# Performance work log

Hardware: AMD Instinct MI355X
Metric: run time of the kernel (lower is better)

Reference implementation:

```python
import jax, jax.numpy as jnp
import numpy as np

T_STEPS, B, I, H = 512, 64, 128, 256
LAST_K, RSIZE = 16, 32


def _xavier(key, shape):
    fan_out, fan_in = shape[0], shape[-1]
    std = (2.0 / (fan_in + fan_out)) ** 0.5
    return (std * jax.random.normal(key, shape)).astype(jnp.float32)


def setup_inputs() -> dict:
    key = jax.random.key(0)
    ks = jax.random.split(key, 8)
    inp = {"x": jax.random.normal(ks[0], (T_STEPS, B, I), dtype=jnp.float32)}
    for n, k in zip(["Wf", "Wi", "Wo", "Wg"], ks[1:5]):
        inp[n + "_w"] = _xavier(k, (H, H + I))
        inp[n + "_b"] = jnp.zeros((H,), jnp.float32)
    inp["Ua_w"] = _xavier(ks[5], (H, H))
    inp["Va_w"] = _xavier(ks[6], (H, H))
    inp["v"] = _xavier(ks[7], (1, H))
    return inp


def _forward(x, Wf_w, Wf_b, Wi_w, Wi_b, Wo_w, Wo_b, Wg_w, Wg_b, Ua_w, Va_w, v):
    T = x.shape[0]
    vv = v[0]  # [H]
    neg_inf = jnp.float32(-jnp.inf)

    def lstm(st, ct, xt):
        inp = jnp.concatenate([st, xt], axis=1)  # [B, H+I], order (hidden, input) as in torch cat((st, x), 1)
        ft = jax.nn.sigmoid(inp @ Wf_w.T + Wf_b)
        it = jax.nn.sigmoid(inp @ Wi_w.T + Wi_b)
        ot = jax.nn.sigmoid(inp @ Wo_w.T + Wo_b)
        gt = jnp.tanh(inp @ Wg_w.T + Wg_b)
        ct = ft * ct + it * gt
        return ot * jnp.tanh(ct), ct

    # ---- step 0 (reset path): st = zero hidden, no attention ----
    st0 = jnp.zeros((B, H), jnp.float32)
    h0, ct0 = lstm(st0, jnp.zeros((B, H), jnp.float32), x[0])
    mem0 = jnp.zeros((LAST_K, B, H), jnp.float32).at[-1].set(h0)  # ring of last_k hiddens (zeros = not yet filled)
    carry0 = (st0, ct0, mem0,
              jnp.zeros((RSIZE, B, H), jnp.float32),   # long_mem buckets
              jnp.full((RSIZE, B), neg_inf),            # long_mask (-inf = empty bucket)
              jnp.zeros((T, B), jnp.float32),           # long_scores (detached accumulator)
              jnp.zeros((B, RSIZE), jnp.float32),       # buck_scores
              jnp.zeros((B,), jnp.int32))               # per-sample bucket fill count

    def body(carry, tx):
        st, ct, mem, long_mem, long_mask, long_scores, buck, fill = carry
        t, xt = tx
        slots = jnp.arange(LAST_K)
        short_valid = slots >= (LAST_K - t)  # slot j holds h_{t-LAST_K+j}; valid iff time >= 0
        # ---- additive attention over short memory + long-term buckets ----
        q = st @ Va_w.T                              # [B,H]
        Uahs = mem @ Ua_w.T                          # [LAST_K,B,H]
        long_uas = long_mem @ Ua_w.T                 # [RSIZE,B,H]
        es = jnp.einsum('kbh,h->kb', jnp.tanh(q[None] + Uahs), vv)
        es = jnp.where(short_valid[:, None], es, neg_inf)
        es_long = jnp.einsum('rbh,h->rb', jnp.tanh(q[None] + long_uas), vv) + long_mask
        alphas = jax.nn.softmax(jnp.concatenate([es, es_long], 0), axis=0)  # [LAST_K+RSIZE,B]
        # accumulate detached attention mass onto absolute-time scores
        det_a = jax.lax.stop_gradient(alphas[:LAST_K])
        times = jnp.clip(t - LAST_K + slots, 0, T - 1)
        long_scores = long_scores.at[times].add(jnp.where(short_valid[:, None], det_a, 0.0))
        comb = jnp.concatenate([mem, long_mem], 0)   # [LAST_K+RSIZE,B,H]
        ct_att = jnp.einsum('nb,nbh->bh', alphas, comb)
        st = 0.5 * (mem[-1] + ct_att)                # comb_hs[-1-rsize] == previous hidden
        # ---- LSTM gating ----
        hidden, ct = lstm(st, ct, xt)
        # ---- bucket insert / argmin-replace (active once t >= LAST_K) ----
        cand = mem[0]                                # h_{t-LAST_K} == memory[0]
        cand_score = jax.lax.stop_gradient(
            jax.lax.dynamic_index_in_dim(long_scores, jnp.clip(t - LAST_K, 0, T - 1), 0, keepdims=False))  # [B]
        minp = jnp.argmin(buck, axis=1)              # [B], first-min like torch.argmin
        min_val = jnp.take_along_axis(buck, minp[:, None], axis=1)[:, 0]
        full = fill >= RSIZE
        addpos = jnp.where(full, minp, fill)
        do_upd = (t >= LAST_K) & (jnp.logical_not(full) | (cand_score > min_val))
        onehot = (jnp.arange(RSIZE)[None, :] == addpos[:, None]) & do_upd[:, None]  # [B,RSIZE]
        sel = onehot.T                               # [RSIZE,B]
        long_mem = jnp.where(sel[:, :, None], cand[None], long_mem)
        long_mask = jnp.where(sel, 0.0, long_mask)
        buck = jnp.where(onehot, cand_score[:, None], buck)
        fill = fill + (do_upd & jnp.logical_not(full)).astype(jnp.int32)
        # ---- push hidden into short-memory ring ----
        mem = jnp.concatenate([mem[1:], hidden[None]], 0)
        return (st, ct, mem, long_mem, long_mask, long_scores, buck, fill), hidden

    ts = jnp.arange(1, T)
    _, hs = jax.lax.scan(jax.checkpoint(body), carry0, (ts, x[1:]))
    return jnp.concatenate([h0[None], hs], 0)  # [T,B,H]


def reference(x, Wf_w, Wf_b, Wi_w, Wi_b, Wo_w, Wo_b, Wg_w, Wg_b, Ua_w, Va_w, v):
    return _forward(x, Wf_w, Wf_b, Wi_w, Wi_b, Wo_w, Wo_b, Wg_w, Wg_b, Ua_w, Va_w, v)
```

## Files before the change

kernel.cpp:

```cpp
#include <hip/hip_runtime.h>
#include <hip/hip_fp16.h>

#define T_STEPS 512
#define NB      64
#define NI      128
#define NH      256
#define LK      16
#define RS      32
#define NS      (LK + RS)

#define WP_OFF   0
#define VAP8_OFF 786432
#define UAP8_OFF 917504
#define LRAW_OFF 1048576
#define LUA_OFF  3145728
#define GX_OFF   5242880
#define WS_NEED  (GX_OFF + (size_t)T_STEPS * NB * NH * 8)

typedef _Float16 half2v __attribute__((ext_vector_type(2)));

__device__ __forceinline__ float hdot(unsigned int w, unsigned int s, float c) {
    return __builtin_amdgcn_fdot2(__builtin_bit_cast(half2v, w),
                                  __builtin_bit_cast(half2v, s), c, false);
}

__device__ __forceinline__ float fsig(float x) {
    return __builtin_amdgcn_rcpf(1.0f + __expf(-x));
}
__device__ __forceinline__ float ftanh(float x) {
    x = fminf(15.0f, fmaxf(-15.0f, x));
    float e = __expf(2.0f * x);
    return (e - 1.0f) * __builtin_amdgcn_rcpf(e + 1.0f);
}

__global__ void prep_weights(const float* __restrict__ Wf, const float* __restrict__ Wi,
                             const float* __restrict__ Wo, const float* __restrict__ Wg,
                             const float* __restrict__ Ua, const float* __restrict__ Va,
                             unsigned char* __restrict__ ws) {
    int e = blockIdx.x * 256 + threadIdx.x;
    if (e < 49152) {
        int h = e & 255, k2 = e >> 8, k = 2 * k2;
        uint4 w; __half2 t;
        t = __floats2half2_rn(Wf[h * 384 + k], Wf[h * 384 + k + 1]); w.x = *(unsigned int*)&t;
        t = __floats2half2_rn(Wi[h * 384 + k], Wi[h * 384 + k + 1]); w.y = *(unsigned int*)&t;
        t = __floats2half2_rn(Wo[h * 384 + k], Wo[h * 384 + k + 1]); w.z = *(unsigned int*)&t;
        t = __floats2half2_rn(Wg[h * 384 + k], Wg[h * 384 + k + 1]); w.w = *(unsigned int*)&t;
        ((uint4*)(ws + WP_OFF))[e] = w;
    } else {
        int e2 = e - 49152;
        const float* S = (e2 < 8192) ? Va : Ua;
        int e3 = e2 & 8191;
        int h = e3 & 255, j = e3 >> 8, k = 8 * j;
        uint4 w; __half2 t;
        t = __floats2half2_rn(S[h * 256 + k + 0], S[h * 256 + k + 1]); w.x = *(unsigned int*)&t;
        t = __floats2half2_rn(S[h * 256 + k + 2], S[h * 256 + k + 3]); w.y = *(unsigned int*)&t;
        t = __floats2half2_rn(S[h * 256 + k + 4], S[h * 256 + k + 5]); w.z = *(unsigned int*)&t;
        t = __floats2half2_rn(S[h * 256 + k + 6], S[h * 256 + k + 7]); w.w = *(unsigned int*)&t;
        ((uint4*)(ws + VAP8_OFF))[e2] = w;
    }
}

__global__ __launch_bounds__(256) void gx_gemm(const float* __restrict__ x,
                                               unsigned char* __restrict__ ws) {
    const int t = blockIdx.x, bg = blockIdx.y, tid = threadIdx.x;
    const uint4* __restrict__ WP = (const uint4*)(ws + WP_OFF);
    uint2* __restrict__ GX = (uint2*)(ws + GX_OFF);
    __shared__ float s_xx[16 * 128];
    const float* xb = x + ((size_t)t * NB + bg * 16) * NI;
#pragma unroll
    for (int r = 0; r < 8; ++r) s_xx[tid + 256 * r] = xb[tid + 256 * r];
    __syncthreads();
    const int h = tid;
    float acc[16][4];
#pragma unroll
    for (int bb = 0; bb < 16; ++bb) { acc[bb][0] = acc[bb][1] = acc[bb][2] = acc[bb][3] = 0.f; }
    for (int k2 = 128; k2 < 192; ++k2) {
        uint4 w = WP[k2 * NH + h];
        float2 wf = __half22float2(*(const __half2*)&w.x);
        float2 wi = __half22float2(*(const __half2*)&w.y);
        float2 wo = __half22float2(*(const __half2*)&w.z);
        float2 wg = __half22float2(*(const __half2*)&w.w);
        int kk = 2 * k2 - 256;
#pragma unroll
        for (int bb = 0; bb < 16; ++bb) {
            float2 xv = *(const float2*)(s_xx + bb * 128 + kk);
            acc[bb][0] += wf.x * xv.x + wf.y * xv.y;
            acc[bb][1] += wi.x * xv.x + wi.y * xv.y;
            acc[bb][2] += wo.x * xv.x + wo.y * xv.y;
            acc[bb][3] += wg.x * xv.x + wg.y * xv.y;
        }
    }
#pragma unroll
    for (int bb = 0; bb < 16; ++bb) {
        __half2 p0 = __floats2half2_rn(acc[bb][0], acc[bb][1]);
        __half2 p1 = __floats2half2_rn(acc[bb][2], acc[bb][3]);
        uint2 u; u.x = *(unsigned int*)&p0; u.y = *(unsigned int*)&p1;
        GX[((size_t)t * NB + bg * 16 + bb) * NH + h] = u;
    }
}

template <int USE_GX>
__global__ __launch_bounds__(1024, 1) void rel_lstm(
    const float* __restrict__ x,
    const float* __restrict__ bf_g, const float* __restrict__ bi_g,
    const float* __restrict__ bo_g, const float* __restrict__ bg_g,
    const float* __restrict__ vv_g,
    unsigned char* __restrict__ ws, float* __restrict__ out) {
    const int tid = threadIdx.x;
    const int b   = blockIdx.x;
    const int wv  = tid >> 6;
    const int ln  = tid & 63;
    const int h16 = (wv << 4) | (ln & 15);
    const int kc  = ln >> 4;

    const uint4* __restrict__ WP   = (const uint4*)(ws + WP_OFF);
    const uint4* __restrict__ VaP8 = (const uint4*)(ws + VAP8_OFF);
    const uint4* __restrict__ UaP8 = (const uint4*)(ws + UAP8_OFF);
    const uint2* __restrict__ GX   = (const uint2*)(ws + GX_OFF);
    float* __restrict__ lraw = (float*)(ws + LRAW_OFF) + b * (RS * NH);
    float* __restrict__ lua  = (float*)(ws + LUA_OFF)  + b * (RS * NH);

    __shared__ __align__(16) _Float16 s_in_h[NH + NI];
    __shared__ __align__(16) _Float16 s_hid_h[NH];
    __shared__ __align__(16) float s_q[NH];
    __shared__ __align__(16) float s_v[NH];
    __shared__ __align__(16) float s_mem[LK][NH];
    __shared__ __align__(16) float s_memua[LK][NH + 8];
    __shared__ float s_es[NS], s_al[NS];
    __shared__ float s_scores[T_STEPS];
    __shared__ float s_mask[RS], s_buck[RS];
    __shared__ float s_minv;
    __shared__ int s_minp, s_fill, s_upd, s_pos;

    for (int i = tid; i < LK * NH; i += 1024) ((float*)s_mem)[i] = 0.f;
    for (int i = tid; i < LK * (NH + 8); i += 1024) ((float*)s_memua)[i] = 0.f;
    if (tid < T_STEPS) s_scores[tid] = 0.f;
    if (tid < NH) s_v[tid] = vv_g[tid];
    if (tid < (NH + NI) / 2) ((unsigned int*)s_in_h)[tid] = 0u;
    if (tid < RS) { s_mask[tid] = -1e30f; s_buck[tid] = 0.f; }
    if (tid == 0) { s_fill = 0; s_upd = 0; s_pos = 0; s_minv = 0.f; s_minp = 0; }
    float bfv = 0.f, biv = 0.f, bov = 0.f, bgv = 0.f;
    if (kc == 0) { bfv = bf_g[h16]; biv = bi_g[h16]; bov = bo_g[h16]; bgv = bg_g[h16]; }
    if (!USE_GX && tid < 64) {
        float2 xv = ((const float2*)(x + (size_t)b * NI))[tid];
        __half2 hx = __floats2half2_rn(xv.x, xv.y);
        ((unsigned int*)s_in_h)[NH / 2 + tid] = *(unsigned int*)&hx;
    }
    float ct = 0.f;
    int base = 0;
    __syncthreads();

    for (int t = 0; t < T_STEPS; ++t) {
        float evA = 0.f, evB = 0.f;
        if (t > 0) {
            {
                const uint4* P   = (wv < 8) ? VaP8 : UaP8;
                const uint4* SRC = (wv < 8) ? (const uint4*)s_in_h : (const uint4*)s_hid_h;
                const int hh = ((wv & 7) << 5) | (ln & 31);
                const int ch = ln >> 5;
                float acc = 0.f;
#pragma unroll 8
                for (int jj = 0; jj < 16; ++jj) {
                    int j = (ch << 4) | jj;
                    uint4 w = P[(j << 8) + hh];
                    uint4 s = SRC[j];
                    acc = hdot(w.x, s.x, acc);
                    acc = hdot(w.y, s.y, acc);
                    acc = hdot(w.z, s.z, acc);
                    acc = hdot(w.w, s.w, acc);
                }
                acc += __shfl_xor(acc, 32, 64);
                if (ch == 0) {
                    if (wv < 8) s_q[hh] = acc;
                    else        s_memua[(base + LK - 1) & (LK - 1)][hh] = acc;
                }
                if (!USE_GX && tid < 64) {
                    float2 xv = ((const float2*)(x + ((size_t)t * NB + b) * NI))[tid];
                    __half2 hx = __floats2half2_rn(xv.x, xv.y);
                    ((unsigned int*)s_in_h)[NH / 2 + tid] = *(unsigned int*)&hx;
                }
            }
            __syncthreads();
            if (tid < 768) {
                const int row = tid >> 4, l = tid & 15;
                bool skip;
                const float* ua;
                if (row < LK) { skip = row < LK - t; ua = s_memua[(base + row) & (LK - 1)]; }
                else          { skip = s_mask[row - LK] < -1e29f; ua = lua + (row - LK) * NH; }
                float esv = -1e30f;
                if (!skip) {
                    float p = 0.f;
#pragma unroll
                    for (int jj = 0; jj < 4; ++jj) {
                        int hh = (l << 2) + (jj << 6);
                        float4 q4 = *(const float4*)(s_q + hh);
                        float4 v4 = *(const float4*)(s_v + hh);
                        float4 u4 = *(const float4*)(ua + hh);
                        p += v4.x * ftanh(q4.x + u4.x);
                        p += v4.y * ftanh(q4.y + u4.y);
                        p += v4.z * ftanh(q4.z + u4.z);
                        p += v4.w * ftanh(q4.w + u4.w);
                    }
                    p += __shfl_xor(p, 1, 16);
                    p += __shfl_xor(p, 2, 16);
                    p += __shfl_xor(p, 4, 16);
                    p += __shfl_xor(p, 8, 16);
                    esv = p;
                }
                if (l == 0) s_es[row] = esv;
            } else if (tid >= 960 && tid < 992) {
                int l = tid - 960;
                float v = s_buck[l]; int idx = l;
#pragma unroll
                for (int off = 1; off < 32; off <<= 1) {
                    float v2 = __shfl_xor(v, off, 32);
                    int  i2 = __shfl_xor(idx, off, 32);
                    if (v2 < v || (v2 == v && i2 < idx)) { v = v2; idx = i2; }
                }
                if (l == 0) { s_minv = v; s_minp = idx; }
            }
            __syncthreads();
            if (tid < 64) {
                float e = (tid < NS) ? s_es[tid] : -1e30f;
                float m = e;
#pragma unroll
                for (int off = 32; off; off >>= 1) m = fmaxf(m, __shfl_xor(m, off, 64));
                float a = (tid < NS) ? __expf(e - m) : 0.f;
                float ssum = a;
#pragma unroll
                for (int off = 32; off; off >>= 1) ssum += __shfl_xor(ssum, off, 64);
                float al = a * __builtin_amdgcn_rcpf(ssum);
                if (tid < NS) s_al[tid] = al;
                float cs = 0.f;
                if (tid < LK) {
                    int time = t - LK + tid;
                    if (time >= 0) {
                        float ns = s_scores[time] + al;
                        s_scores[time] = ns;
                        cs = ns;
                    }
                }
                if (tid == 0) {
                    int upd = 0, pos = 0;
                    if (t >= LK) {
                        int fill = s_fill;
                        bool full = fill >= RS;
                        upd = (!full) || (cs > s_minv);
                        pos = full ? s_minp : fill;
                        if (upd) { s_mask[pos] = 0.f; s_buck[pos] = cs; if (!full) s_fill = fill + 1; }
                    }
                    s_upd = upd; s_pos = pos;
                }
            }
            __syncthreads();
            {
                float catt = 0.f;
                const int n0 = kc * 12;
#pragma unroll
                for (int n = n0; n < n0 + 12; ++n) {
                    float a = s_al[n];
                    if (n < LK) catt += a * s_mem[(base + n) & (LK - 1)][h16];
                    else if (a != 0.f) catt += a * lraw[(n - LK) * NH + h16];
                }
                catt += __shfl_xor(catt, 16, 64);
                catt += __shfl_xor(catt, 32, 64);
                if (kc == 1 && s_upd) {
                    int p0 = base & (LK - 1);
                    evA = s_mem[p0][h16];
                    evB = s_memua[p0][h16];
                }
                if (kc == 0) {
                    float stv = 0.5f * (s_mem[(base + LK - 1) & (LK - 1)][h16] + catt);
                    s_in_h[h16] = (_Float16)stv;
                }
            }
            __syncthreads();
        }
        {
            uint2 gx = {0u, 0u};
            if (USE_GX && kc == 0) gx = GX[((size_t)t * NB + b) * NH + h16];
            constexpr int KP = USE_GX ? 32 : 48;
            const unsigned int* S2 = (const unsigned int*)s_in_h;
            float af = 0.f, ai = 0.f, ao = 0.f, ag = 0.f;
            const int lo = kc * KP;
#pragma unroll 8
            for (int k2 = lo; k2 < lo + KP; ++k2) {
                uint4 w = WP[(k2 << 8) + h16];
                unsigned int s2 = S2[k2];
                af = hdot(w.x, s2, af);
                ai = hdot(w.y, s2, ai);
                ao = hdot(w.z, s2, ao);
                ag = hdot(w.w, s2, ag);
            }
            af += __shfl_xor(af, 16, 64); af += __shfl_xor(af, 32, 64);
            ai += __shfl_xor(ai, 16, 64); ai += __shfl_xor(ai, 32, 64);
            ao += __shfl_xor(ao, 16, 64); ao += __shfl_xor(ao, 32, 64);
            ag += __shfl_xor(ag, 16, 64); ag += __shfl_xor(ag, 32, 64);
            if (kc == 0) {
                float pf = af + bfv, pi = ai + biv, po = ao + bov, pg = ag + bgv;
                if (USE_GX) {
                    float2 fi = __half22float2(*(const __half2*)&gx.x);
                    float2 og = __half22float2(*(const __half2*)&gx.y);
                    pf += fi.x; pi += fi.y; po += og.x; pg += og.y;
                }
                float f  = fsig(pf);
                float ii = fsig(pi);
                float o  = fsig(po);
                float g  = ftanh(pg);
                ct = f * ct + ii * g;
                float hid = o * ftanh(ct);
                out[((size_t)t * NB + b) * NH + h16] = hid;
                s_mem[base & (LK - 1)][h16] = hid;
                s_hid_h[h16] = (_Float16)hid;
            } else if (kc == 1 && s_upd) {
                lraw[s_pos * NH + h16] = evA;
                lua[s_pos * NH + h16]  = evB;
            }
        }
        base++;
        __syncthreads();
    }
}

extern "C" void kernel_launch(void* const* d_in, const int* in_sizes, int n_in,
                              void* d_out, int out_size, void* d_ws, size_t ws_size,
                              hipStream_t stream) {
    const float* x  = (const float*)d_in[0];
    const float* Wf = (const float*)d_in[1];
    const float* bf = (const float*)d_in[2];
    const float* Wi = (const float*)d_in[3];
    const float* bi = (const float*)d_in[4];
    const float* Wo = (const float*)d_in[5];
    const float* bo = (const float*)d_in[6];
    const float* Wg = (const float*)d_in[7];
    const float* bg = (const float*)d_in[8];
    const float* Ua = (const float*)d_in[9];
    const float* Va = (const float*)d_in[10];
    const float* vv = (const float*)d_in[11];
    unsigned char* ws = (unsigned char*)d_ws;
    float* out = (float*)d_out;

    prep_weights<<<256, 256, 0, stream>>>(Wf, Wi, Wo, Wg, Ua, Va, ws);
    if (ws_size >= WS_NEED) {
        gx_gemm<<<dim3(T_STEPS, 4), 256, 0, stream>>>(x, ws);
        rel_lstm<1><<<NB, 1024, 0, stream>>>(x, bf, bi, bo, bg, vv, ws, out);
    } else {
        rel_lstm<0><<<NB, 1024, 0, stream>>>(x, bf, bi, bo, bg, vv, ws, out);
    }
}
```

Before: 5.917 ms.

## Move long-memory buffers to LDS and compute softmax redundantly per wave

The per-block long-memory buffers (raw hiddens and their Ua projections) move from global workspace into shared memory, so the attention score and context reads no longer go to global memory. Every wave now computes the softmax itself and broadcasts the weights through shuffles. This removes the s_al array and one block-wide barrier per timestep. The GX prefetch and eviction-candidate reads are also hoisted earlier so their latency overlaps other work. The cost is 64KB more LDS, redundant softmax work in all 16 waves, and a fully unrolled projection loop.

```diff
diff --git a/kernel.cpp b/kernel.cpp
--- a/kernel.cpp
+++ b/kernel.cpp
@@ -12,8 +12,6 @@
 #define WP_OFF   0
 #define VAP8_OFF 786432
 #define UAP8_OFF 917504
-#define LRAW_OFF 1048576
-#define LUA_OFF  3145728
 #define GX_OFF   5242880
 #define WS_NEED  (GX_OFF + (size_t)T_STEPS * NB * NH * 8)
 
@@ -117,8 +115,6 @@
     const uint4* __restrict__ VaP8 = (const uint4*)(ws + VAP8_OFF);
     const uint4* __restrict__ UaP8 = (const uint4*)(ws + UAP8_OFF);
     const uint2* __restrict__ GX   = (const uint2*)(ws + GX_OFF);
-    float* __restrict__ lraw = (float*)(ws + LRAW_OFF) + b * (RS * NH);
-    float* __restrict__ lua  = (float*)(ws + LUA_OFF)  + b * (RS * NH);
 
     __shared__ __align__(16) _Float16 s_in_h[NH + NI];
     __shared__ __align__(16) _Float16 s_hid_h[NH];
@@ -126,7 +122,9 @@
     __shared__ __align__(16) float s_v[NH];
     __shared__ __align__(16) float s_mem[LK][NH];
     __shared__ __align__(16) float s_memua[LK][NH + 8];
-    __shared__ float s_es[NS], s_al[NS];
+    __shared__ __align__(16) float s_lraw[RS * NH];
+    __shared__ __align__(16) float s_lua[RS * NH];
+    __shared__ float s_es[NS];
     __shared__ float s_scores[T_STEPS];
     __shared__ float s_mask[RS], s_buck[RS];
     __shared__ float s_minv;
@@ -134,6 +132,7 @@
 
     for (int i = tid; i < LK * NH; i += 1024) ((float*)s_mem)[i] = 0.f;
     for (int i = tid; i < LK * (NH + 8); i += 1024) ((float*)s_memua)[i] = 0.f;
+    for (int i = tid; i < RS * NH; i += 1024) { s_lraw[i] = 0.f; s_lua[i] = 0.f; }
     if (tid < T_STEPS) s_scores[tid] = 0.f;
     if (tid < NH) s_v[tid] = vv_g[tid];
     if (tid < (NH + NI) / 2) ((unsigned int*)s_in_h)[tid] = 0u;
@@ -152,6 +151,8 @@
 
     for (int t = 0; t < T_STEPS; ++t) {
         float evA = 0.f, evB = 0.f;
+        uint2 gx = {0u, 0u};
+        if (USE_GX && kc == 0) gx = GX[((size_t)t * NB + b) * NH + h16];
         if (t > 0) {
             {
                 const uint4* P   = (wv < 8) ? VaP8 : UaP8;
@@ -159,7 +160,7 @@
                 const int hh = ((wv & 7) << 5) | (ln & 31);
                 const int ch = ln >> 5;
                 float acc = 0.f;
-#pragma unroll 8
+#pragma unroll
                 for (int jj = 0; jj < 16; ++jj) {
                     int j = (ch << 4) | jj;
                     uint4 w = P[(j << 8) + hh];
@@ -174,6 +175,11 @@
                     if (wv < 8) s_q[hh] = acc;
                     else        s_memua[(base + LK - 1) & (LK - 1)][hh] = acc;
                 }
+                if (kc == 1) {
+                    int p0 = base & (LK - 1);
+                    evA = s_mem[p0][h16];
+                    evB = s_memua[p0][h16];
+                }
                 if (!USE_GX && tid < 64) {
                     float2 xv = ((const float2*)(x + ((size_t)t * NB + b) * NI))[tid];
                     __half2 hx = __floats2half2_rn(xv.x, xv.y);
@@ -186,7 +192,7 @@
                 bool skip;
                 const float* ua;
                 if (row < LK) { skip = row < LK - t; ua = s_memua[(base + row) & (LK - 1)]; }
-                else          { skip = s_mask[row - LK] < -1e29f; ua = lua + (row - LK) * NH; }
+                else          { skip = s_mask[row - LK] < -1e29f; ua = s_lua + (row - LK) * NH; }
                 float esv = -1e30f;
                 if (!skip) {
                     float p = 0.f;
@@ -220,55 +226,48 @@
                 if (l == 0) { s_minv = v; s_minp = idx; }
             }
             __syncthreads();
-            if (tid < 64) {
-                float e = (tid < NS) ? s_es[tid] : -1e30f;
+            {
+                float e = (ln < NS) ? s_es[ln] : -1e30f;
                 float m = e;
 #pragma unroll
                 for (int off = 32; off; off >>= 1) m = fmaxf(m, __shfl_xor(m, off, 64));
-                float a = (tid < NS) ? __expf(e - m) : 0.f;
+                float a = (ln < NS) ? __expf(e - m) : 0.f;
                 float ssum = a;
 #pragma unroll
                 for (int off = 32; off; off >>= 1) ssum += __shfl_xor(ssum, off, 64);
                 float al = a * __builtin_amdgcn_rcpf(ssum);
-                if (tid < NS) s_al[tid] = al;
-                float cs = 0.f;
-                if (tid < LK) {
-                    int time = t - LK + tid;
-                    if (time >= 0) {
-                        float ns = s_scores[time] + al;
-                        s_scores[time] = ns;
-                        cs = ns;
+                if (wv == 0) {
+                    float cs = 0.f;
+                    if (ln < LK) {
+                        int time = t - LK + ln;
+                        if (time >= 0) {
+                            float ns = s_scores[time] + al;
+                            s_scores[time] = ns;
+                            cs = ns;
+                        }
                     }
-                }
-                if (tid == 0) {
-                    int upd = 0, pos = 0;
-                    if (t >= LK) {
-                        int fill = s_fill;
-                        bool full = fill >= RS;
-                        upd = (!full) || (cs > s_minv);
-                        pos = full ? s_minp : fill;
-                        if (upd) { s_mask[pos] = 0.f; s_buck[pos] = cs; if (!full) s_fill = fill + 1; }
+                    if (ln == 0) {
+                        int upd = 0, pos = 0;
+                        if (t >= LK) {
+                            int fill = s_fill;
+                            bool full = fill >= RS;
+                            upd = (!full) || (cs > s_minv);
+                            pos = full ? s_minp : fill;
+                            if (upd) { s_mask[pos] = 0.f; s_buck[pos] = cs; if (!full) s_fill = fill + 1; }
+                        }
+                        s_upd = upd; s_pos = pos;
                     }
-                    s_upd = upd; s_pos = pos;
-                }
-            }
-            __syncthreads();
-            {
+                }
                 float catt = 0.f;
                 const int n0 = kc * 12;
 #pragma unroll
                 for (int n = n0; n < n0 + 12; ++n) {
-                    float a = s_al[n];
-                    if (n < LK) catt += a * s_mem[(base + n) & (LK - 1)][h16];
-                    else if (a != 0.f) catt += a * lraw[(n - LK) * NH + h16];
+                    float a2 = __shfl(al, n);
+                    if (n < LK) catt += a2 * s_mem[(base + n) & (LK - 1)][h16];
+                    else if (a2 != 0.f) catt += a2 * s_lraw[(n - LK) * NH + h16];
                 }
                 catt += __shfl_xor(catt, 16, 64);
                 catt += __shfl_xor(catt, 32, 64);
-                if (kc == 1 && s_upd) {
-                    int p0 = base & (LK - 1);
-                    evA = s_mem[p0][h16];
-                    evB = s_memua[p0][h16];
-                }
                 if (kc == 0) {
                     float stv = 0.5f * (s_mem[(base + LK - 1) & (LK - 1)][h16] + catt);
                     s_in_h[h16] = (_Float16)stv;
@@ -277,8 +276,6 @@
             __syncthreads();
         }
         {
-            uint2 gx = {0u, 0u};
-            if (USE_GX && kc == 0) gx = GX[((size_t)t * NB + b) * NH + h16];
             constexpr int KP = USE_GX ? 32 : 48;
             const unsigned int* S2 = (const unsigned int*)s_in_h;
             float af = 0.f, ai = 0.f, ao = 0.f, ag = 0.f;
@@ -313,8 +310,8 @@
                 s_mem[base & (LK - 1)][h16] = hid;
                 s_hid_h[h16] = (_Float16)hid;
             } else if (kc == 1 && s_upd) {
-                lraw[s_pos * NH + h16] = evA;
-                lua[s_pos * NH + h16]  = evB;
+                s_lraw[s_pos * NH + h16] = evA;
+                s_lua[s_pos * NH + h16]  = evB;
             }
         }
         base++;
```

New measurement: 6.094 ms. 1.03x slower.

## Keep long-memory buckets in LDS, prefetch GX early, use nontemporal weight loads

Applied to the files above, without the earlier changes.

Moves the per-sample long-memory bucket arrays (raw hiddens and their Ua projections) from global workspace into shared memory. This removes global-memory round trips inside the sequential per-step critical path. It also issues the GX gate-input load at the top of each step so its latency overlaps the attention phase, and hoists the evicted-slot reads earlier. Weight loads switch to nontemporal loads. The cost is about 64KB of extra LDS per block, which must still fit, and a cache-policy change on weight reads that are reused every step.

```diff
diff --git a/kernel.cpp b/kernel.cpp
--- a/kernel.cpp
+++ b/kernel.cpp
@@ -12,12 +12,23 @@
 #define WP_OFF   0
 #define VAP8_OFF 786432
 #define UAP8_OFF 917504
-#define LRAW_OFF 1048576
-#define LUA_OFF  3145728
 #define GX_OFF   5242880
 #define WS_NEED  (GX_OFF + (size_t)T_STEPS * NB * NH * 8)
 
 typedef _Float16 half2v __attribute__((ext_vector_type(2)));
+typedef unsigned int u32x4 __attribute__((ext_vector_type(4)));
+typedef unsigned int u32x2 __attribute__((ext_vector_type(2)));
+
+__device__ __forceinline__ u32x4 ntl4(const void* p) {
+    return __builtin_nontemporal_load((const u32x4*)p);
+}
+__device__ __forceinline__ u32x2 ntl2(const void* p) {
+    return __builtin_nontemporal_load((const u32x2*)p);
+}
+__device__ __forceinline__ float2 h2f2(unsigned int u) {
+    __half2 h = *(__half2*)&u;
+    return __half22float2(h);
+}
 
 __device__ __forceinline__ float hdot(unsigned int w, unsigned int s, float c) {
     return __builtin_amdgcn_fdot2(__builtin_bit_cast(half2v, w),
@@ -117,8 +128,6 @@
     const uint4* __restrict__ VaP8 = (const uint4*)(ws + VAP8_OFF);
     const uint4* __restrict__ UaP8 = (const uint4*)(ws + UAP8_OFF);
     const uint2* __restrict__ GX   = (const uint2*)(ws + GX_OFF);
-    float* __restrict__ lraw = (float*)(ws + LRAW_OFF) + b * (RS * NH);
-    float* __restrict__ lua  = (float*)(ws + LUA_OFF)  + b * (RS * NH);
 
     __shared__ __align__(16) _Float16 s_in_h[NH + NI];
     __shared__ __align__(16) _Float16 s_hid_h[NH];
@@ -126,6 +135,8 @@
     __shared__ __align__(16) float s_v[NH];
     __shared__ __align__(16) float s_mem[LK][NH];
     __shared__ __align__(16) float s_memua[LK][NH + 8];
+    __shared__ __align__(16) float s_lraw[RS * NH];
+    __shared__ __align__(16) float s_lua[RS * NH];
     __shared__ float s_es[NS], s_al[NS];
     __shared__ float s_scores[T_STEPS];
     __shared__ float s_mask[RS], s_buck[RS];
@@ -134,6 +145,7 @@
 
     for (int i = tid; i < LK * NH; i += 1024) ((float*)s_mem)[i] = 0.f;
     for (int i = tid; i < LK * (NH + 8); i += 1024) ((float*)s_memua)[i] = 0.f;
+    for (int i = tid; i < RS * NH; i += 1024) { s_lraw[i] = 0.f; s_lua[i] = 0.f; }
     if (tid < T_STEPS) s_scores[tid] = 0.f;
     if (tid < NH) s_v[tid] = vv_g[tid];
     if (tid < (NH + NI) / 2) ((unsigned int*)s_in_h)[tid] = 0u;
@@ -152,6 +164,8 @@
 
     for (int t = 0; t < T_STEPS; ++t) {
         float evA = 0.f, evB = 0.f;
+        u32x2 gx = {0u, 0u};
+        if (USE_GX && kc == 0) gx = ntl2(&GX[((size_t)t * NB + b) * NH + h16]);
         if (t > 0) {
             {
                 const uint4* P   = (wv < 8) ? VaP8 : UaP8;
@@ -162,7 +176,7 @@
 #pragma unroll 8
                 for (int jj = 0; jj < 16; ++jj) {
                     int j = (ch << 4) | jj;
-                    uint4 w = P[(j << 8) + hh];
+                    u32x4 w = ntl4(&P[(j << 8) + hh]);
                     uint4 s = SRC[j];
                     acc = hdot(w.x, s.x, acc);
                     acc = hdot(w.y, s.y, acc);
@@ -173,6 +187,11 @@
                 if (ch == 0) {
                     if (wv < 8) s_q[hh] = acc;
                     else        s_memua[(base + LK - 1) & (LK - 1)][hh] = acc;
+                }
+                if (kc == 1) {
+                    int p0 = base & (LK - 1);
+                    evA = s_mem[p0][h16];
+                    evB = s_memua[p0][h16];
                 }
                 if (!USE_GX && tid < 64) {
                     float2 xv = ((const float2*)(x + ((size_t)t * NB + b) * NI))[tid];
@@ -186,7 +205,7 @@
                 bool skip;
                 const float* ua;
                 if (row < LK) { skip = row < LK - t; ua = s_memua[(base + row) & (LK - 1)]; }
-                else          { skip = s_mask[row - LK] < -1e29f; ua = lua + (row - LK) * NH; }
+                else          { skip = s_mask[row - LK] < -1e29f; ua = s_lua + (row - LK) * NH; }
                 float esv = -1e30f;
                 if (!skip) {
                     float p = 0.f;
@@ -260,15 +279,10 @@
                 for (int n = n0; n < n0 + 12; ++n) {
                     float a = s_al[n];
                     if (n < LK) catt += a * s_mem[(base + n) & (LK - 1)][h16];
-                    else if (a != 0.f) catt += a * lraw[(n - LK) * NH + h16];
+                    else if (a != 0.f) catt += a * s_lraw[(n - LK) * NH + h16];
                 }
                 catt += __shfl_xor(catt, 16, 64);
                 catt += __shfl_xor(catt, 32, 64);
-                if (kc == 1 && s_upd) {
-                    int p0 = base & (LK - 1);
-                    evA = s_mem[p0][h16];
-                    evB = s_memua[p0][h16];
-                }
                 if (kc == 0) {
                     float stv = 0.5f * (s_mem[(base + LK - 1) & (LK - 1)][h16] + catt);
                     s_in_h[h16] = (_Float16)stv;
@@ -277,15 +291,13 @@
             __syncthreads();
         }
         {
-            uint2 gx = {0u, 0u};
-            if (USE_GX && kc == 0) gx = GX[((size_t)t * NB + b) * NH + h16];
             constexpr int KP = USE_GX ? 32 : 48;
             const unsigned int* S2 = (const unsigned int*)s_in_h;
             float af = 0.f, ai = 0.f, ao = 0.f, ag = 0.f;
             const int lo = kc * KP;
 #pragma unroll 8
             for (int k2 = lo; k2 < lo + KP; ++k2) {
-                uint4 w = WP[(k2 << 8) + h16];
+                u32x4 w = ntl4(&WP[(k2 << 8) + h16]);
                 unsigned int s2 = S2[k2];
                 af = hdot(w.x, s2, af);
                 ai = hdot(w.y, s2, ai);
@@ -299,8 +311,8 @@
             if (kc == 0) {
                 float pf = af + bfv, pi = ai + biv, po = ao + bov, pg = ag + bgv;
                 if (USE_GX) {
-                    float2 fi = __half22float2(*(const __half2*)&gx.x);
-                    float2 og = __half22float2(*(const __half2*)&gx.y);
+                    float2 fi = h2f2(gx.x);
+                    float2 og = h2f2(gx.y);
                     pf += fi.x; pi += fi.y; po += og.x; pg += og.y;
                 }
                 float f  = fsig(pf);
@@ -313,8 +325,8 @@
                 s_mem[base & (LK - 1)][h16] = hid;
                 s_hid_h[h16] = (_Float16)hid;
             } else if (kc == 1 && s_upd) {
-                lraw[s_pos * NH + h16] = evA;
-                lua[s_pos * NH + h16]  = evB;
+                s_lraw[s_pos * NH + h16] = evA;
+                s_lua[s_pos * NH + h16]  = evB;
             }
         }
         base++;
```

Result: slower. 10.72 ms (+81.1%).
